# Kernel tuning notes

Measured on AMD Instinct MI355X. Metric: run time of the kernel, lower is better.

## Reference

```python
import jax, jax.numpy as jnp
import numpy as np

D = 300      # dim_in (hardcoded in HGConv)
N_CAT = 3    # n_categories
M = 16384    # nodes
E = 4096     # hyperedges


def setup_inputs() -> dict:
    key = jax.random.key(0)
    ks = jax.random.split(key, 11)
    s = 1.0 / np.sqrt(D)
    u = lambda k, shape: jax.random.uniform(k, shape, jnp.float32, -s, s)
    return {
        "node_feats": jax.random.normal(ks[0], (M, D), jnp.float32),
        "edge_feats": jax.random.normal(ks[1], (E, D), jnp.float32),
        "inc_mat": jax.random.uniform(ks[2], (M, E), jnp.float32),
        # VertexConv params (Linear weights stored as (in, out); torch stores transpose)
        "W_att": u(ks[3], (D, D)),       # attention, no bias
        "W_proj": u(ks[4], (D, D)),      # projection, no bias
        "alpha": jnp.array(0.5, jnp.float32),
        # HypergraphEdgeAggregation params
        "ec_W_att": u(ks[5], (D, 1)),    # attention, no bias
        "ec_W_proj": u(ks[6], (D, D)),
        "ec_b_proj": u(ks[7], (D,)),
        # final classifier
        "fc_W": u(ks[8], (D, N_CAT)),
        "fc_b": u(ks[9], (N_CAT,)),
    }


def reference(node_feats, edge_feats, inc_mat, W_att, W_proj, alpha,
              ec_W_att, ec_W_proj, ec_b_proj, fc_W, fc_b):
    # --- VertexConv ---
    # edge attention scores: inc^T @ (X @ W_att)  -> (e, d)
    edge_att = inc_mat.T @ (node_feats @ W_att)
    attn = jax.nn.softmax(edge_att, axis=1)
    # fused equivalent of einsum('me,md->med') then einsum('med,ed->ed'):
    # edge_feat[e,d] = (inc^T @ X)[e,d] * attn[e,d]
    ef = (inc_mat.T @ node_feats) * attn
    ef = ef @ W_proj
    ef = alpha * edge_feats + (1.0 - alpha) * ef          # residual mix
    # --- HypergraphEdgeAggregation ---
    scores = ef @ ec_W_att                                # (e, 1)
    w = jax.nn.softmax(scores, axis=0)                    # softmax over edges
    pooled = jnp.sum(ef * w, axis=0)                      # (d,)
    out = pooled @ ec_W_proj + ec_b_proj                  # (d,)
    # --- classifier (LogSoftmax is defined but NOT applied in forward) ---
    logits = out @ fc_W + fc_b                            # (n_categories,)
    return logits
```

## Files before the change

kernel.cpp:

```cpp
#include <hip/hip_runtime.h>
#include <math.h>

typedef _Float16 f16;
typedef _Float16 f16x8 __attribute__((ext_vector_type(8)));
typedef _Float16 f16x4 __attribute__((ext_vector_type(4)));
typedef __fp16 fp16x2 __attribute__((ext_vector_type(2)));
typedef float f32x4 __attribute__((ext_vector_type(4)));
typedef float f32x16 __attribute__((ext_vector_type(16)));

#define NM 16384
#define NE 4096
#define ND 300
#define DP 320
#define PS 1310720

__device__ __forceinline__ int swz(int r) { return (r ^ (r >> 2)) & 3; }

#define GLOAD_LDS16(gsrc, ldst)                                              \
  __builtin_amdgcn_global_load_lds(                                          \
      (__attribute__((address_space(1))) void*)(gsrc),                       \
      (__attribute__((address_space(3))) void*)(ldst), 16, 0, 0)

__global__ void k0_wt(const float* __restrict__ Watt, f16* __restrict__ WT) {
  int idx = blockIdx.x * 256 + threadIdx.x;
  if (idx >= DP * DP) return;
  int j = idx / DP, d = idx % DP;
  float v = (j < ND && d < ND) ? Watt[d * ND + j] : 0.f;
  WT[(size_t)j * DP + d] = (f16)v;
}

__global__ __launch_bounds__(256) void k1a_xprep(const float* __restrict__ X,
                                                 f16* __restrict__ XT) {
  __shared__ f16 tile[64][324];
  int m0 = blockIdx.x * 64;
  for (int idx = threadIdx.x; idx < 64 * 80; idx += 256) {
    int m = idx / 80, q = idx % 80;
    int d = q * 4;
    float4 v = make_float4(0.f, 0.f, 0.f, 0.f);
    if (d < ND) v = *(const float4*)(X + (size_t)(m0 + m) * ND + d);
    tile[m][d] = (f16)v.x; tile[m][d + 1] = (f16)v.y;
    tile[m][d + 2] = (f16)v.z; tile[m][d + 3] = (f16)v.w;
  }
  __syncthreads();
  for (int idx = threadIdx.x; idx < DP * 8; idx += 256) {
    int d = idx >> 3, part = idx & 7;
    f16x8 hv;
#pragma unroll
    for (int i = 0; i < 8; ++i) hv[i] = tile[part * 8 + i][d];
    *(f16x8*)(XT + (size_t)d * NM + m0 + part * 8) = hv;
  }
}

#define K2WAIT(N) asm volatile("s_waitcnt vmcnt(" #N ") lgkmcnt(0)" ::: "memory")
#define K2BAR()                                        \
  do {                                                 \
    asm volatile("" ::: "memory");                     \
    __builtin_amdgcn_s_barrier();                      \
    asm volatile("" ::: "memory");                     \
  } while (0)

__global__ __launch_bounds__(256, 2) void k2_bigmm(const float* __restrict__ inc,
                                                   const f16* __restrict__ XT,
                                                   f16* __restrict__ Zp) {
  constexpr int STEPS = 32;
  __shared__ __align__(16) char lds[57344];
  const int t = threadIdx.x, lane = t & 63, wid = t >> 6;
  const int bx = blockIdx.x;
  const int kb = (bx & 7) | (((bx >> 3) & 1) << 3);
  const int eb = bx >> 4;
  const int e0 = eb * 128;
  const size_t kbase = (size_t)kb * 1024;
  f16* __restrict__ Zout = Zp + (size_t)kb * PS;

  const int we = wid >> 1, wj = wid & 1;
  const int l31 = lane & 31, oct = lane >> 5;
  int sl[2];
#pragma unroll
  for (int kk = 0; kk < 2; ++kk)
    sl[kk] = (((kk * 2 + oct) ^ ((l31 >> 1) & 3)) & 3) << 4;
  const int arow = (we * 64 + l31) * 64;
  const int brow = (wj * 160 + l31) * 64;
  const int ep = t & 63, kq = t >> 6;
  const int sA = (kq ^ ((ep >> 1) & 3)) & 3;
  const int wa0 = 40960 + ep * 64 + sA * 16;
  const int wa1 = 40960 + (ep + 64) * 64 + sA * 16;
  const float* pA = inc + (kbase + kq * 8) * NE + e0 + ep;
  const int br = wid * 80 + (lane >> 2);
  const f16* pB = XT + (size_t)br * NM + kbase + 8 * ((lane & 3) ^ ((lane >> 3) & 3));

  float rAx[8], rAy[8];
  f32x16 acc[2][5];
#pragma unroll
  for (int me = 0; me < 2; ++me)
#pragma unroll
    for (int f = 0; f < 5; ++f)
#pragma unroll
      for (int r = 0; r < 16; ++r) acc[me][f][r] = 0.f;

#define LOADA(RX, RY)                                                          \
  {                                                                            \
    _Pragma("unroll") for (int i = 0; i < 8; ++i) {                            \
      RX[i] = pA[(size_t)i * NE];                                              \
      RY[i] = pA[(size_t)i * NE + 64];                                         \
    }                                                                          \
    pA += (size_t)32 * NE;                                                     \
  }
#define DMAB(S)                                                                \
  {                                                                            \
    _Pragma("unroll") for (int i = 0; i < 5; ++i) {                            \
      GLOAD_LDS16(pB + (size_t)(i * 16) * NM,                                  \
                  lds + (S)*20480 + wid * 5120 + i * 1024);                    \
    }                                                                          \
    pB += 32;                                                                  \
  }
#define WRITEA(RX, RY, S)                                                      \
  {                                                                            \
    union { fp16x2 h; uint32_t u; } ux_[4], uy_[4];                            \
    _Pragma("unroll") for (int z = 0; z < 4; ++z) {                            \
      ux_[z].h = __builtin_amdgcn_cvt_pkrtz(RX[2 * z], RX[2 * z + 1]);         \
      uy_[z].h = __builtin_amdgcn_cvt_pkrtz(RY[2 * z], RY[2 * z + 1]);         \
    }                                                                          \
    *(uint4*)(lds + wa0 + (S)*8192) =                                          \
        make_uint4(ux_[0].u, ux_[1].u, ux_[2].u, ux_[3].u);                    \
    *(uint4*)(lds + wa1 + (S)*8192) =                                          \
        make_uint4(uy_[0].u, uy_[1].u, uy_[2].u, uy_[3].u);                    \
  }
#define COMPUTE(S)                                                             \
  {                                                                            \
    __builtin_amdgcn_s_setprio(1);                                             \
    _Pragma("unroll") for (int kk = 0; kk < 2; ++kk) {                         \
      f16x8 a0_ = *(const f16x8*)(lds + 40960 + (S)*8192 + arow + sl[kk]);     \
      f16x8 a1_ = *(const f16x8*)(lds + 40960 + (S)*8192 + arow + 2048 + sl[kk]); \
      _Pragma("unroll") for (int f = 0; f < 5; ++f) {                          \
        f16x8 b_ = *(const f16x8*)(lds + (S)*20480 + brow + f * 2048 + sl[kk]); \
        acc[0][f] = __builtin_amdgcn_mfma_f32_32x32x16_f16(a0_, b_, acc[0][f], 0, 0, 0); \
        acc[1][f] = __builtin_amdgcn_mfma_f32_32x32x16_f16(a1_, b_, acc[1][f], 0, 0, 0); \
      }                                                                        \
    }                                                                          \
    __builtin_amdgcn_s_setprio(0);                                             \
  }

  LOADA(rAx, rAy);
  DMAB(0);
  WRITEA(rAx, rAy, 0);
  LOADA(rAx, rAy);
  DMAB(1);
  K2WAIT(21);
  K2BAR();

  for (int tt = 0; tt < STEPS - 2; ++tt) {
    COMPUTE(tt & 1);
    K2BAR();
    WRITEA(rAx, rAy, (tt + 1) & 1);
    LOADA(rAx, rAy);
    DMAB(tt & 1);
    K2WAIT(21);
    K2BAR();
  }
  COMPUTE(0);
  K2BAR();
  WRITEA(rAx, rAy, 1);
  K2WAIT(0);
  K2BAR();
  COMPUTE(1);

#pragma unroll
  for (int me = 0; me < 2; ++me)
#pragma unroll
    for (int f = 0; f < 5; ++f) {
      int jg = wj * 160 + f * 32 + l31;
      int ebase = e0 + we * 64 + me * 32 + 4 * oct;
#pragma unroll
      for (int r = 0; r < 16; ++r) {
        int eg = ebase + (r & 3) + 8 * (r >> 2);
        Zout[(size_t)eg * DP + jg] = (f16)acc[me][f][r];
      }
    }
#undef LOADA
#undef DMAB
#undef WRITEA
}

__global__ __launch_bounds__(256) void k2s_sum(const f16* __restrict__ Zp,
                                               f16* __restrict__ EF0) {
  const int idx = (blockIdx.x * 256 + threadIdx.x) * 4;
  float s0 = 0.f, s1 = 0.f, s2 = 0.f, s3 = 0.f;
#pragma unroll
  for (int i = 0; i < 16; ++i) {
    f16x4 v = *(const f16x4*)(Zp + (size_t)i * PS + idx);
    s0 += (float)v[0]; s1 += (float)v[1]; s2 += (float)v[2]; s3 += (float)v[3];
  }
  f16x4 o;
  o[0] = (f16)s0; o[1] = (f16)s1; o[2] = (f16)s2; o[3] = (f16)s3;
  *(f16x4*)(EF0 + idx) = o;
}

__global__ __launch_bounds__(256, 1) void k2b_att(const f16* __restrict__ EF0,
                                                  const f16* __restrict__ WT,
                                                  float* __restrict__ att) {
  constexpr int STEPS = 10;
  __shared__ __align__(16) char lds[57344];
  const int t = threadIdx.x, lane = t & 63, wid = t >> 6;
  const int e0 = blockIdx.x * 128;
  const int we = wid >> 1, wj = wid & 1;
  const int l31 = lane & 31, oct = lane >> 5;
  int sl[2];
#pragma unroll
  for (int kk = 0; kk < 2; ++kk)
    sl[kk] = (((kk * 2 + oct) ^ ((l31 >> 1) & 3)) & 3) << 4;
  const int arow = (we * 64 + l31) * 64;
  const int brow = (wj * 160 + l31) * 64;
  const int srcsw = 8 * ((lane & 3) ^ ((lane >> 3) & 3));
  const f16* pA = EF0 + (size_t)(e0 + wid * 32 + (lane >> 2)) * DP + srcsw;
  const f16* pB = WT + (size_t)(wid * 80 + (lane >> 2)) * DP + srcsw;

  f32x16 acc[2][5];
#pragma unroll
  for (int me = 0; me < 2; ++me)
#pragma unroll
    for (int f = 0; f < 5; ++f)
#pragma unroll
      for (int r = 0; r < 16; ++r) acc[me][f][r] = 0.f;

#define STAGE2(S)                                                              \
  {                                                                            \
    _Pragma("unroll") for (int i = 0; i < 2; ++i) {                            \
      GLOAD_LDS16(pA + (size_t)(i * 16) * DP,                                  \
                  lds + 40960 + (S)*8192 + wid * 2048 + i * 1024);             \
    }                                                                          \
    pA += 32;                                                                  \
    _Pragma("unroll") for (int i = 0; i < 5; ++i) {                            \
      GLOAD_LDS16(pB + (size_t)(i * 16) * DP,                                  \
                  lds + (S)*20480 + wid * 5120 + i * 1024);                    \
    }                                                                          \
    pB += 32;                                                                  \
  }

  STAGE2(0);
  STAGE2(1);
  K2WAIT(7);
  K2BAR();
  for (int tt = 0; tt < STEPS - 2; ++tt) {
    COMPUTE(tt & 1);
    K2BAR();
    STAGE2(tt & 1);
    K2WAIT(7);
    K2BAR();
  }
  COMPUTE(0);
  K2BAR();
  K2WAIT(0);
  COMPUTE(1);

#pragma unroll
  for (int me = 0; me < 2; ++me)
#pragma unroll
    for (int f = 0; f < 5; ++f) {
      int jg = wj * 160 + f * 32 + l31;
      int ebase = e0 + we * 64 + me * 32 + 4 * oct;
#pragma unroll
      for (int r = 0; r < 16; ++r) {
        int eg = ebase + (r & 3) + 8 * (r >> 2);
        att[(size_t)eg * DP + jg] = acc[me][f][r];
      }
    }
#undef STAGE2
#undef COMPUTE
}

__global__ __launch_bounds__(256) void k3_edge(const float* __restrict__ att,
                                               const f16* __restrict__ EF0,
                                               const float* __restrict__ edge_feats,
                                               const float* __restrict__ Wproj,
                                               const float* __restrict__ alphaP,
                                               const float* __restrict__ ecWatt,
                                               float* __restrict__ ef,
                                               float* __restrict__ scores) {
  __shared__ float efw[16][304];
  const int t = threadIdx.x, lane = t & 63, w = t >> 6;
  const int e0 = blockIdx.x * 16;
  for (int el = 0; el < 4; ++el) {
    int e = e0 + w * 4 + el;
    const size_t ro = (size_t)e * DP;
    float p[5];
    float mx = -1e30f;
#pragma unroll
    for (int u = 0; u < 5; ++u) {
      int d = u * 64 + lane;
      p[u] = (d < ND) ? att[ro + d] : -1e30f;
      mx = fmaxf(mx, p[u]);
    }
    for (int o = 32; o; o >>= 1) mx = fmaxf(mx, __shfl_xor(mx, o));
    float s = 0.f;
#pragma unroll
    for (int u = 0; u < 5; ++u) {
      int d = u * 64 + lane;
      float pe = (d < ND) ? expf(p[u] - mx) : 0.f;
      p[u] = pe;
      s += pe;
    }
    for (int o = 32; o; o >>= 1) s += __shfl_xor(s, o);
    float inv = 1.f / s;
#pragma unroll
    for (int u = 0; u < 5; ++u) {
      int d = u * 64 + lane;
      if (d < 304)
        efw[w * 4 + el][d] = (d < ND) ? (float)EF0[ro + d] * p[u] * inv : 0.f;
    }
  }
  __syncthreads();
  const int jl = lane & 15, kc = lane >> 4;
  const float alpha = alphaP[0];
  float acc[4][19];
#pragma unroll
  for (int ei = 0; ei < 4; ++ei)
#pragma unroll
    for (int jj = 0; jj < 19; ++jj) acc[ei][jj] = 0.f;
  const int d0 = kc * 75;
  const float* efw0 = &efw[w * 4 + 0][0];
  const float* efw1 = &efw[w * 4 + 1][0];
  const float* efw2 = &efw[w * 4 + 2][0];
  const float* efw3 = &efw[w * 4 + 3][0];
  for (int dd = 0; dd < 75; ++dd) {
    int d = d0 + dd;
    const float* wr = Wproj + (size_t)d * ND + jl;
    float w0 = efw0[d], w1 = efw1[d], w2 = efw2[d], w3 = efw3[d];
#pragma unroll
    for (int jj = 0; jj < 19; ++jj) {
      int j = jl + jj * 16;
      float wv = (j < ND) ? wr[jj * 16] : 0.f;
      acc[0][jj] += w0 * wv;
      acc[1][jj] += w1 * wv;
      acc[2][jj] += w2 * wv;
      acc[3][jj] += w3 * wv;
    }
  }
#pragma unroll
  for (int ei = 0; ei < 4; ++ei)
#pragma unroll
    for (int jj = 0; jj < 19; ++jj) {
      acc[ei][jj] += __shfl_xor(acc[ei][jj], 16);
      acc[ei][jj] += __shfl_xor(acc[ei][jj], 32);
    }
  float scp[4] = {0.f, 0.f, 0.f, 0.f};
#pragma unroll
  for (int ei = 0; ei < 4; ++ei) {
    int e = e0 + w * 4 + ei;
#pragma unroll
    for (int jj = 0; jj < 19; ++jj) {
      int j = jl + jj * 16;
      float v = 0.f;
      if (j < ND) {
        v = alpha * edge_feats[(size_t)e * ND + j] + (1.f - alpha) * acc[ei][jj];
        scp[ei] += v * ecWatt[j];
      }
      if (kc == 0) ef[(size_t)e * 304 + j] = v;
    }
  }
#pragma unroll
  for (int ei = 0; ei < 4; ++ei)
    for (int o = 8; o; o >>= 1) scp[ei] += __shfl_xor(scp[ei], o);
  if (lane == 0) {
#pragma unroll
    for (int ei = 0; ei < 4; ++ei) scores[e0 + w * 4 + ei] = scp[ei];
  }
}

__global__ __launch_bounds__(1024) void k4a_softmax(const float* __restrict__ scores,
                                                    float* __restrict__ w) {
  __shared__ float red[16];
  __shared__ float red2[16];
  const int t = threadIdx.x, lane = t & 63, wv = t >> 6;
  float v[4];
  float mx = -1e30f;
#pragma unroll
  for (int u = 0; u < 4; ++u) {
    v[u] = scores[t + u * 1024];
    mx = fmaxf(mx, v[u]);
  }
  for (int o = 32; o; o >>= 1) mx = fmaxf(mx, __shfl_xor(mx, o));
  if (lane == 0) red[wv] = mx;
  __syncthreads();
  float m2 = red[0];
  for (int i = 1; i < 16; ++i) m2 = fmaxf(m2, red[i]);
  float s = 0.f;
#pragma unroll
  for (int u = 0; u < 4; ++u) {
    v[u] = expf(v[u] - m2);
    s += v[u];
  }
  for (int o = 32; o; o >>= 1) s += __shfl_xor(s, o);
  if (lane == 0) red2[wv] = s;
  __syncthreads();
  float S = 0.f;
  for (int i = 0; i < 16; ++i) S += red2[i];
  float inv = 1.f / S;
#pragma unroll
  for (int u = 0; u < 4; ++u) w[t + u * 1024] = v[u] * inv;
}

__global__ __launch_bounds__(256) void k4b_pool(const float* __restrict__ ef,
                                                const float* __restrict__ w,
                                                float* __restrict__ partial) {
  const int b = blockIdx.x, t = threadIdx.x;
  const int e0 = b * 64;
  for (int j = t; j < 304; j += 256) {
    float acc = 0.f;
    for (int e = 0; e < 64; ++e) acc += w[e0 + e] * ef[(size_t)(e0 + e) * 304 + j];
    partial[b * 304 + j] = acc;
  }
}

__global__ __launch_bounds__(256) void k4c_final(const float* __restrict__ partial,
                                                 const float* __restrict__ ecWp,
                                                 const float* __restrict__ ecb,
                                                 const float* __restrict__ fcW,
                                                 const float* __restrict__ fcb,
                                                 float* __restrict__ out) {
  __shared__ float pooled[304];
  __shared__ float o[304];
  const int t = threadIdx.x;
  for (int j = t; j < 304; j += 256) {
    float acc = 0.f;
    for (int b = 0; b < 64; ++b) acc += partial[b * 304 + j];
    pooled[j] = acc;
  }
  __syncthreads();
  for (int j2 = t; j2 < ND; j2 += 256) {
    float acc = ecb[j2];
    for (int j = 0; j < ND; ++j) acc += pooled[j] * ecWp[j * ND + j2];
    o[j2] = acc;
  }
  __syncthreads();
  if (t < 3) {
    float acc = fcb[t];
    for (int j2 = 0; j2 < ND; ++j2) acc += o[j2] * fcW[j2 * 3 + t];
    out[t] = acc;
  }
}

extern "C" void kernel_launch(void* const* d_in, const int* in_sizes, int n_in,
                              void* d_out, int out_size, void* d_ws, size_t ws_size,
                              hipStream_t stream) {
  const float* X = (const float*)d_in[0];
  const float* EFEATS = (const float*)d_in[1];
  const float* INC = (const float*)d_in[2];
  const float* WATT = (const float*)d_in[3];
  const float* WPROJ = (const float*)d_in[4];
  const float* ALPHA = (const float*)d_in[5];
  const float* ECATT = (const float*)d_in[6];
  const float* ECWP = (const float*)d_in[7];
  const float* ECB = (const float*)d_in[8];
  const float* FCW = (const float*)d_in[9];
  const float* FCB = (const float*)d_in[10];

  char* ws = (char*)d_ws;
  f16* XT = (f16*)(ws);
  f16* Zp = (f16*)(ws + 10485760);
  f16* WT = (f16*)(ws + 52428800);
  f16* EF0 = (f16*)(ws + 52633600);
  float* att = (float*)(ws + 55255040);
  float* ef = (float*)(ws + 60497920);
  float* sc = (float*)(ws + 65478656);
  float* wv = (float*)(ws + 65495040);
  float* pp = (float*)(ws + 65511424);

  hipLaunchKernelGGL(k0_wt, dim3(400), dim3(256), 0, stream, WATT, WT);
  hipLaunchKernelGGL(k1a_xprep, dim3(256), dim3(256), 0, stream, X, XT);
  hipLaunchKernelGGL(k2_bigmm, dim3(512), dim3(256), 0, stream, INC, XT, Zp);
  hipLaunchKernelGGL(k2s_sum, dim3(1280), dim3(256), 0, stream, Zp, EF0);
  hipLaunchKernelGGL(k2b_att, dim3(32), dim3(256), 0, stream, EF0, WT, att);
  hipLaunchKernelGGL(k3_edge, dim3(256), dim3(256), 0, stream, att, EF0, EFEATS,
                     WPROJ, ALPHA, ECATT, ef, sc);
  hipLaunchKernelGGL(k4a_softmax, dim3(1), dim3(1024), 0, stream, sc, wv);
  hipLaunchKernelGGL(k4b_pool, dim3(64), dim3(256), 0, stream, ef, wv, pp);
  hipLaunchKernelGGL(k4c_final, dim3(1), dim3(256), 0, stream, pp, ECWP, ECB, FCW,
                     FCB, (float*)d_out);
}
```

Baseline: 252.1 us.

## Merge prep kernels, fuse softmax into pooling, double-buffer A registers in bigmm

Merges the W transpose and X transpose-convert kernels into one launch, and folds the edge softmax into the pooling kernel so each block recomputes the global max and sum itself. The big GEMM main loop is unrolled by two with ping-pong register buffers for A, so the next global load is issued before the previous tile is written to LDS. The final kernel gets a wider block and a wave-shuffle reduction for the classifier. The aim is fewer launches and more overlap of A loads with compute, at the cost of more registers in the GEMM and redundant softmax reductions across 64 blocks.

```diff
diff --git a/kernel.cpp b/kernel.cpp
--- a/kernel.cpp
+++ b/kernel.cpp
@@ -21,33 +21,37 @@
       (__attribute__((address_space(1))) void*)(gsrc),                       \
       (__attribute__((address_space(3))) void*)(ldst), 16, 0, 0)
 
-__global__ void k0_wt(const float* __restrict__ Watt, f16* __restrict__ WT) {
-  int idx = blockIdx.x * 256 + threadIdx.x;
-  if (idx >= DP * DP) return;
-  int j = idx / DP, d = idx % DP;
-  float v = (j < ND && d < ND) ? Watt[d * ND + j] : 0.f;
-  WT[(size_t)j * DP + d] = (f16)v;
-}
-
-__global__ __launch_bounds__(256) void k1a_xprep(const float* __restrict__ X,
-                                                 f16* __restrict__ XT) {
+__global__ __launch_bounds__(256) void k01_prep(const float* __restrict__ X,
+                                                const float* __restrict__ Watt,
+                                                f16* __restrict__ XT,
+                                                f16* __restrict__ WT) {
   __shared__ f16 tile[64][324];
-  int m0 = blockIdx.x * 64;
-  for (int idx = threadIdx.x; idx < 64 * 80; idx += 256) {
-    int m = idx / 80, q = idx % 80;
-    int d = q * 4;
-    float4 v = make_float4(0.f, 0.f, 0.f, 0.f);
-    if (d < ND) v = *(const float4*)(X + (size_t)(m0 + m) * ND + d);
-    tile[m][d] = (f16)v.x; tile[m][d + 1] = (f16)v.y;
-    tile[m][d + 2] = (f16)v.z; tile[m][d + 3] = (f16)v.w;
-  }
-  __syncthreads();
-  for (int idx = threadIdx.x; idx < DP * 8; idx += 256) {
-    int d = idx >> 3, part = idx & 7;
-    f16x8 hv;
-#pragma unroll
-    for (int i = 0; i < 8; ++i) hv[i] = tile[part * 8 + i][d];
-    *(f16x8*)(XT + (size_t)d * NM + m0 + part * 8) = hv;
+  const int bx = blockIdx.x;
+  if (bx < 256) {
+    int m0 = bx * 64;
+    for (int idx = threadIdx.x; idx < 64 * 80; idx += 256) {
+      int m = idx / 80, q = idx % 80;
+      int d = q * 4;
+      float4 v = make_float4(0.f, 0.f, 0.f, 0.f);
+      if (d < ND) v = *(const float4*)(X + (size_t)(m0 + m) * ND + d);
+      tile[m][d] = (f16)v.x; tile[m][d + 1] = (f16)v.y;
+      tile[m][d + 2] = (f16)v.z; tile[m][d + 3] = (f16)v.w;
+    }
+    __syncthreads();
+    for (int idx = threadIdx.x; idx < DP * 8; idx += 256) {
+      int d = idx >> 3, part = idx & 7;
+      f16x8 hv;
+#pragma unroll
+      for (int i = 0; i < 8; ++i) hv[i] = tile[part * 8 + i][d];
+      *(f16x8*)(XT + (size_t)d * NM + m0 + part * 8) = hv;
+    }
+  } else {
+    int idx = (bx - 256) * 256 + threadIdx.x;
+    if (idx < DP * DP) {
+      int j = idx / DP, d = idx % DP;
+      float v = (j < ND && d < ND) ? Watt[d * ND + j] : 0.f;
+      WT[(size_t)j * DP + d] = (f16)v;
+    }
   }
 }
 
@@ -62,7 +66,6 @@
 __global__ __launch_bounds__(256, 2) void k2_bigmm(const float* __restrict__ inc,
                                                    const f16* __restrict__ XT,
                                                    f16* __restrict__ Zp) {
-  constexpr int STEPS = 32;
   __shared__ __align__(16) char lds[57344];
   const int t = threadIdx.x, lane = t & 63, wid = t >> 6;
   const int bx = blockIdx.x;
@@ -88,7 +91,7 @@
   const int br = wid * 80 + (lane >> 2);
   const f16* pB = XT + (size_t)br * NM + kbase + 8 * ((lane & 3) ^ ((lane >> 3) & 3));
 
-  float rAx[8], rAy[8];
+  float rAx0[8], rAy0[8], rAx1[8], rAy1[8];
   f32x16 acc[2][5];
 #pragma unroll
   for (int me = 0; me < 2; ++me)
@@ -140,26 +143,33 @@
     __builtin_amdgcn_s_setprio(0);                                             \
   }
 
-  LOADA(rAx, rAy);
+  LOADA(rAx0, rAy0);
   DMAB(0);
-  WRITEA(rAx, rAy, 0);
-  LOADA(rAx, rAy);
+  WRITEA(rAx0, rAy0, 0);
+  LOADA(rAx0, rAy0);
   DMAB(1);
   K2WAIT(21);
   K2BAR();
 
-  for (int tt = 0; tt < STEPS - 2; ++tt) {
-    COMPUTE(tt & 1);
-    K2BAR();
-    WRITEA(rAx, rAy, (tt + 1) & 1);
-    LOADA(rAx, rAy);
-    DMAB(tt & 1);
+  for (int it = 0; it < 15; ++it) {
+    COMPUTE(0);
+    K2BAR();
+    LOADA(rAx1, rAy1);
+    DMAB(0);
+    WRITEA(rAx0, rAy0, 1);
+    K2WAIT(21);
+    K2BAR();
+    COMPUTE(1);
+    K2BAR();
+    LOADA(rAx0, rAy0);
+    DMAB(1);
+    WRITEA(rAx1, rAy1, 0);
     K2WAIT(21);
     K2BAR();
   }
   COMPUTE(0);
   K2BAR();
-  WRITEA(rAx, rAy, 1);
+  WRITEA(rAx0, rAy0, 1);
   K2WAIT(0);
   K2BAR();
   COMPUTE(1);
@@ -366,52 +376,43 @@
   }
 }
 
-__global__ __launch_bounds__(1024) void k4a_softmax(const float* __restrict__ scores,
-                                                    float* __restrict__ w) {
-  __shared__ float red[16];
-  __shared__ float red2[16];
-  const int t = threadIdx.x, lane = t & 63, wv = t >> 6;
-  float v[4];
+__global__ __launch_bounds__(256) void k4ab_pool(const float* __restrict__ sc,
+                                                 const float* __restrict__ ef,
+                                                 float* __restrict__ pp) {
+  __shared__ float redm[4];
+  __shared__ float reds[4];
+  __shared__ float wsh[64];
+  const int t = threadIdx.x, lane = t & 63, w = t >> 6;
+  float v[16];
   float mx = -1e30f;
 #pragma unroll
-  for (int u = 0; u < 4; ++u) {
-    v[u] = scores[t + u * 1024];
+  for (int u = 0; u < 16; ++u) {
+    v[u] = sc[t + u * 256];
     mx = fmaxf(mx, v[u]);
   }
   for (int o = 32; o; o >>= 1) mx = fmaxf(mx, __shfl_xor(mx, o));
-  if (lane == 0) red[wv] = mx;
-  __syncthreads();
-  float m2 = red[0];
-  for (int i = 1; i < 16; ++i) m2 = fmaxf(m2, red[i]);
+  if (lane == 0) redm[w] = mx;
+  __syncthreads();
+  float m2 = fmaxf(fmaxf(redm[0], redm[1]), fmaxf(redm[2], redm[3]));
   float s = 0.f;
 #pragma unroll
-  for (int u = 0; u < 4; ++u) {
-    v[u] = expf(v[u] - m2);
-    s += v[u];
-  }
+  for (int u = 0; u < 16; ++u) s += expf(v[u] - m2);
   for (int o = 32; o; o >>= 1) s += __shfl_xor(s, o);
-  if (lane == 0) red2[wv] = s;
-  __syncthreads();
-  float S = 0.f;
-  for (int i = 0; i < 16; ++i) S += red2[i];
-  float inv = 1.f / S;
-#pragma unroll
-  for (int u = 0; u < 4; ++u) w[t + u * 1024] = v[u] * inv;
-}
-
-__global__ __launch_bounds__(256) void k4b_pool(const float* __restrict__ ef,
-                                                const float* __restrict__ w,
-                                                float* __restrict__ partial) {
-  const int b = blockIdx.x, t = threadIdx.x;
-  const int e0 = b * 64;
+  if (lane == 0) reds[w] = s;
+  __syncthreads();
+  float inv = 1.f / (reds[0] + reds[1] + reds[2] + reds[3]);
+  const int e0 = blockIdx.x * 64;
+  if (t < 64) wsh[t] = expf(sc[e0 + t] - m2) * inv;
+  __syncthreads();
   for (int j = t; j < 304; j += 256) {
     float acc = 0.f;
-    for (int e = 0; e < 64; ++e) acc += w[e0 + e] * ef[(size_t)(e0 + e) * 304 + j];
-    partial[b * 304 + j] = acc;
-  }
-}
-
-__global__ __launch_bounds__(256) void k4c_final(const float* __restrict__ partial,
+#pragma unroll 8
+    for (int e = 0; e < 64; ++e) acc += wsh[e] * ef[(size_t)(e0 + e) * 304 + j];
+    pp[blockIdx.x * 304 + j] = acc;
+  }
+}
+
+__global__ __launch_bounds__(320) void k4c_final(const float* __restrict__ pp,
                                                  const float* __restrict__ ecWp,
                                                  const float* __restrict__ ecb,
                                                  const float* __restrict__ fcW,
@@ -420,22 +421,28 @@
   __shared__ float pooled[304];
   __shared__ float o[304];
   const int t = threadIdx.x;
-  for (int j = t; j < 304; j += 256) {
+  if (t < 304) {
     float acc = 0.f;
-    for (int b = 0; b < 64; ++b) acc += partial[b * 304 + j];
-    pooled[j] = acc;
-  }
-  __syncthreads();
-  for (int j2 = t; j2 < ND; j2 += 256) {
-    float acc = ecb[j2];
-    for (int j = 0; j < ND; ++j) acc += pooled[j] * ecWp[j * ND + j2];
-    o[j2] = acc;
-  }
-  __syncthreads();
-  if (t < 3) {
-    float acc = fcb[t];
-    for (int j2 = 0; j2 < ND; ++j2) acc += o[j2] * fcW[j2 * 3 + t];
-    out[t] = acc;
+#pragma unroll 8
+    for (int b = 0; b < 64; ++b) acc += pp[b * 304 + t];
+    pooled[t] = acc;
+  }
+  __syncthreads();
+  if (t < ND) {
+    float acc = ecb[t];
+#pragma unroll 4
+    for (int j = 0; j < ND; ++j) acc += pooled[j] * ecWp[(size_t)j * ND + t];
+    o[t] = acc;
+  }
+  __syncthreads();
+  if (t < 64) {
+#pragma unroll
+    for (int c = 0; c < 3; ++c) {
+      float a = 0.f;
+      for (int j2 = t; j2 < ND; j2 += 64) a += o[j2] * fcW[j2 * 3 + c];
+      for (int off = 32; off; off >>= 1) a += __shfl_xor(a, off);
+      if (t == 0) out[c] = a + fcb[c];
+    }
   }
 }
 
@@ -462,18 +469,15 @@
   float* att = (float*)(ws + 55255040);
   float* ef = (float*)(ws + 60497920);
   float* sc = (float*)(ws + 65478656);
-  float* wv = (float*)(ws + 65495040);
-  float* pp = (float*)(ws + 65511424);
-
-  hipLaunchKernelGGL(k0_wt, dim3(400), dim3(256), 0, stream, WATT, WT);
-  hipLaunchKernelGGL(k1a_xprep, dim3(256), dim3(256), 0, stream, X, XT);
+  float* pp = (float*)(ws + 65495040);
+
+  hipLaunchKernelGGL(k01_prep, dim3(656), dim3(256), 0, stream, X, WATT, XT, WT);
   hipLaunchKernelGGL(k2_bigmm, dim3(512), dim3(256), 0, stream, INC, XT, Zp);
   hipLaunchKernelGGL(k2s_sum, dim3(1280), dim3(256), 0, stream, Zp, EF0);
   hipLaunchKernelGGL(k2b_att, dim3(32), dim3(256), 0, stream, EF0, WT, att);
   hipLaunchKernelGGL(k3_edge, dim3(256), dim3(256), 0, stream, att, EF0, EFEATS,
                      WPROJ, ALPHA, ECATT, ef, sc);
-  hipLaunchKernelGGL(k4a_softmax, dim3(1), dim3(1024), 0, stream, sc, wv);
-  hipLaunchKernelGGL(k4b_pool, dim3(64), dim3(256), 0, stream, ef, wv, pp);
-  hipLaunchKernelGGL(k4c_final, dim3(1), dim3(256), 0, stream, pp, ECWP, ECB, FCW,
+  hipLaunchKernelGGL(k4ab_pool, dim3(64), dim3(256), 0, stream, sc, ef, pp);
+  hipLaunchKernelGGL(k4c_final, dim3(1), dim3(320), 0, stream, pp, ECWP, ECB, FCW,
                      FCB, (float*)d_out);
 }
```

After: 245.1 us. 2.8% less time.
